# Kernel tuning notes

Hardware: AMD Instinct MI355X
Metric: run time of the kernel (lower is better)

The kernel has to match this reference:

```python
import jax, jax.numpy as jnp
import numpy as np
import math

_DENSE_LOCAL_W = 64
_DYADIC = [96, 128, 192, 256, 384, 512, 768, 1024, 1536]
OFFSETS = sorted(set(range(0, _DENSE_LOCAL_W + 1)) | set(_DYADIC))  # 74 offsets

B, N, D, H = 1, 2048, 1024, 16
HD = D // H


def setup_inputs() -> dict:
    key = jax.random.key(0)
    ks = jax.random.split(key, 8)
    s = 1.0 / math.sqrt(D)
    x = jax.random.normal(ks[0], (B, N, D), dtype=jnp.float32)
    Wqkv = jax.random.uniform(ks[1], (3 * D, D), jnp.float32, -s, s)
    bqkv = jax.random.uniform(ks[2], (3 * D,), jnp.float32, -s, s)
    Wgate = jax.random.uniform(ks[3], (D, D), jnp.float32, -s, s)
    bgate = jax.random.uniform(ks[4], (D,), jnp.float32, -s, s)
    Wout = jax.random.uniform(ks[5], (D, D), jnp.float32, -s, s)
    bout = jax.random.uniform(ks[6], (D,), jnp.float32, -s, s)
    # pos_bias init exactly as in the module: -log(1+delta) * alpha_h, shape (O, H)
    alphas = jnp.linspace(0.2, 2.0, H)
    deltas = jnp.array([math.log(1.0 + d) for d in OFFSETS], dtype=jnp.float32)
    pos_bias = -deltas[:, None] * alphas[None, :]
    offsets = jnp.array(OFFSETS, dtype=jnp.int32)
    return {"x": x, "Wqkv": Wqkv, "bqkv": bqkv, "Wgate": Wgate, "bgate": bgate,
            "Wout": Wout, "bout": bout, "pos_bias": pos_bias, "offsets": offsets}


def reference(x, Wqkv, bqkv, Wgate, bgate, Wout, bout, pos_bias, offsets):
    Bx, Nx, Dx = x.shape
    qkv = x @ Wqkv.T + bqkv                       # (B, N, 3D)
    q, k, v = jnp.split(qkv, 3, axis=-1)
    q = q.reshape(Bx, Nx, H, HD).transpose(0, 2, 1, 3)  # (B, H, N, HD)
    k = k.reshape(Bx, Nx, H, HD).transpose(0, 2, 1, 3)
    v = v.reshape(Bx, Nx, H, HD).transpose(0, 2, 1, 3)
    scale = HD ** -0.5

    # gather shifted K/V: position n attends to n - delta for each fixed offset
    n_idx = jnp.arange(Nx, dtype=jnp.int32)[:, None]      # (N, 1)
    idx = n_idx - offsets[None, :]                        # (N, O)
    valid = idx >= 0                                      # (N, O)
    idx_c = jnp.clip(idx, 0, Nx - 1)
    K_all = k[:, :, idx_c, :]                             # (B, H, N, O, HD)
    V_all = v[:, :, idx_c, :]

    scores = jnp.einsum('bhnd,bhnod->bhno', q, K_all) * scale
    scores = scores + pos_bias.T[None, :, None, :]        # (1, H, 1, O)
    scores = jnp.where(valid[None, None], scores, -jnp.inf)
    alpha = jax.nn.softmax(scores, axis=-1)               # (B, H, N, O)
    out = jnp.einsum('bhno,bhnod->bhnd', alpha, V_all)    # (B, H, N, HD)

    flat = out.transpose(0, 2, 1, 3).reshape(Bx, Nx, Dx)  # (B, N, D)
    gate = jax.nn.sigmoid(x @ Wgate.T + bgate)
    return (flat * gate) @ Wout.T + bout                  # dropout = identity (eval)
```

## Files before the change

### kernel.cpp

```cpp
#include <hip/hip_runtime.h>
#include <hip/hip_bf16.h>

#define SEQ_N 2048
#define DIM   1024
#define NHEAD 16
#define HDIM  64
#define LDQ   4096
#define NOFF  74
#define NDENSE 65
#define NJ    224
#define NT    16
#define PST   232
#define QST   88

typedef __attribute__((ext_vector_type(8)))  __bf16 bv8;
typedef __attribute__((ext_vector_type(4)))  __bf16 bv4;
typedef __attribute__((ext_vector_type(4)))  float  f32x4;
typedef __attribute__((ext_vector_type(16))) float  f32x16;

typedef __attribute__((address_space(3))) void as3_void;
typedef __attribute__((address_space(1))) void as1_void;

__device__ __forceinline__ void async16(const void* g, void* l) {
  __builtin_amdgcn_global_load_lds((as1_void*)(unsigned long long)g,
                                   (as3_void*)l, 16, 0, 0);
}

#define E1 (SEQ_N * DIM)
#define E2 (E1 + 3 * DIM * DIM)
#define E3 (E2 + DIM * DIM)
#define E4 (E3 + DIM * DIM)
__global__ __launch_bounds__(256) void cvt_all(
    const float* __restrict__ x, const float* __restrict__ wqkv,
    const float* __restrict__ wgate, const float* __restrict__ wout,
    __bf16* __restrict__ dst) {
  long i = ((long)blockIdx.x * 256 + threadIdx.x) * 8;
  if (i >= E4) return;
  const float* s; long o;
  if (i < E1)      { s = x;     o = i; }
  else if (i < E2) { s = wqkv;  o = i - E1; }
  else if (i < E3) { s = wgate; o = i - E2; }
  else             { s = wout;  o = i - E3; }
  float4 v0 = *(const float4*)(s + o);
  float4 v1 = *(const float4*)(s + o + 4);
  bv8 ov;
  ov[0] = (__bf16)v0.x; ov[1] = (__bf16)v0.y; ov[2] = (__bf16)v0.z; ov[3] = (__bf16)v0.w;
  ov[4] = (__bf16)v1.x; ov[5] = (__bf16)v1.y; ov[6] = (__bf16)v1.z; ov[7] = (__bf16)v1.w;
  *(bv8*)(dst + i) = ov;
}

template <int BM_, int BN_, int KT, int GX, int GY, typename OutT>
__global__ __launch_bounds__(256, 4) void gemm_bt(
    const __bf16* __restrict__ A, const __bf16* __restrict__ B1,
    const __bf16* __restrict__ B2, const float* __restrict__ bias1,
    const float* __restrict__ bias2, int Nsplit,
    OutT* __restrict__ C, int ldc, int K) {
  __shared__ __attribute__((aligned(16))) __bf16 Asm[BM_ * KT];
  __shared__ __attribute__((aligned(16))) __bf16 Bsm[BN_ * KT];
  constexpr int NI   = BM_ / 64;
  constexpr int NJ32 = BN_ / 64;
  constexpr int CA = BM_ * KT / 8;
  constexpr int CB = BN_ * KT / 8;
  constexpr int CPR = KT / 8;

  const int tid  = threadIdx.x;
  const int lane = tid & 63;
  const int wave = tid >> 6;
  const int wr = wave >> 1, wc = wave & 1;
  const int m31 = lane & 31;
  const int h1  = lane >> 5;
  const int l7  = lane & 7;

  constexpr int NWG = GX * GY;
  const int bid  = blockIdx.y * GX + blockIdx.x;
  const int work = (bid & 7) * (NWG >> 3) + (bid >> 3);
  const int bn0 = (work / GY) * BN_;
  const int bm0 = (work % GY) * BM_;

  const __bf16* Bp;
  const float* biasp;
  if (bn0 < Nsplit) { Bp = B1 + (size_t)bn0 * K;            biasp = bias1 + bn0; }
  else              { Bp = B2 + (size_t)(bn0 - Nsplit) * K; biasp = bias2 + (bn0 - Nsplit); }
  const __bf16* Ap = A + (size_t)bm0 * K;

  f32x16 acc[NI][NJ32] = {};

  for (int kt = 0; kt < K; kt += KT) {
    __syncthreads();
#pragma unroll
    for (int c0 = 0; c0 < CA + CB; c0 += 256) {
      int c = c0 + tid;
      if (c < CA) {
        int rr = c / CPR, qq = c % CPR;
        int qs = qq ^ (rr & 7);
        async16(Ap + (size_t)rr * K + kt + qs * 8, Asm + c * 8);
      } else {
        int cb = c - CA;
        int rr = cb / CPR, qq = cb % CPR;
        int qs = qq ^ (rr & 7);
        async16(Bp + (size_t)rr * K + kt + qs * 8, Bsm + cb * 8);
      }
    }
    __syncthreads();

#pragma unroll
    for (int kk = 0; kk < KT / 16; ++kk) {
      const int qs = ((kk * 2 + h1) ^ l7) * 8;
      bv8 af[NI], bfr[NJ32];
#pragma unroll
      for (int i = 0; i < NI; ++i)
        af[i] = *(const bv8*)(Asm + (wr * (BM_ / 2) + i * 32 + m31) * KT + qs);
#pragma unroll
      for (int j = 0; j < NJ32; ++j)
        bfr[j] = *(const bv8*)(Bsm + (wc * (BN_ / 2) + j * 32 + m31) * KT + qs);
#pragma unroll
      for (int i = 0; i < NI; ++i)
#pragma unroll
        for (int j = 0; j < NJ32; ++j)
          acc[i][j] = __builtin_amdgcn_mfma_f32_32x32x16_bf16(af[i], bfr[j], acc[i][j], 0, 0, 0);
    }
  }

#pragma unroll
  for (int i = 0; i < NI; ++i) {
#pragma unroll
    for (int j = 0; j < NJ32; ++j) {
      int ccol = wc * (BN_ / 2) + j * 32 + m31;
      float b = biasp[ccol];
#pragma unroll
      for (int reg = 0; reg < 16; ++reg) {
        int row = bm0 + wr * (BM_ / 2) + i * 32 + (reg & 3) + 8 * (reg >> 2) + 4 * h1;
        C[(size_t)row * ldc + bn0 + ccol] = (OutT)(acc[i][j][reg] + b);
      }
    }
  }
}

#define BKT 128

template <int GX, int GY, typename OutT>
__global__ __launch_bounds__(256) void gemm_bt64(
    const __bf16* __restrict__ A, const __bf16* __restrict__ B,
    const float* __restrict__ bias, OutT* __restrict__ C, int ldc, int K) {
  __shared__ __attribute__((aligned(16))) __bf16 Asm[64 * BKT];
  __shared__ __attribute__((aligned(16))) __bf16 Bsm[64 * BKT];
  constexpr int CM = 64 * BKT / 8;
  constexpr int CPR = BKT / 8;

  const int tid  = threadIdx.x;
  const int lane = tid & 63;
  const int wave = tid >> 6;
  const int wr = wave >> 1, wc = wave & 1;
  const int m31 = lane & 31;
  const int h1  = lane >> 5;
  const int l7  = lane & 7;

  constexpr int NWG = GX * GY;
  const int bid  = blockIdx.y * GX + blockIdx.x;
  const int work = (bid & 7) * (NWG >> 3) + (bid >> 3);
  const int bn0 = (work / GY) * 64;
  const int bm0 = (work % GY) * 64;

  const __bf16* Ap = A + (size_t)bm0 * K;
  const __bf16* Bp = B + (size_t)bn0 * K;
  const float* biasp = bias + bn0;

  f32x16 acc = {};

  for (int kt = 0; kt < K; kt += BKT) {
    __syncthreads();
#pragma unroll
    for (int c0 = 0; c0 < CM; c0 += 256) {
      int c = c0 + tid;
      int rr = c / CPR, qq = c % CPR;
      int qs = qq ^ (rr & 7);
      async16(Ap + (size_t)rr * K + kt + qs * 8, Asm + c * 8);
      async16(Bp + (size_t)rr * K + kt + qs * 8, Bsm + c * 8);
    }
    __syncthreads();

#pragma unroll
    for (int kk = 0; kk < BKT / 16; ++kk) {
      const int qs = ((kk * 2 + h1) ^ l7) * 8;
      bv8 a = *(const bv8*)(Asm + (wr * 32 + m31) * BKT + qs);
      bv8 b = *(const bv8*)(Bsm + (wc * 32 + m31) * BKT + qs);
      acc = __builtin_amdgcn_mfma_f32_32x32x16_bf16(a, b, acc, 0, 0, 0);
    }
  }

  {
    int ccol = wc * 32 + m31;
    float b = biasp[ccol];
#pragma unroll
    for (int reg = 0; reg < 16; ++reg) {
      int row = bm0 + wr * 32 + (reg & 3) + 8 * (reg >> 2) + 4 * h1;
      C[(size_t)row * ldc + bn0 + ccol] = (OutT)(acc[reg] + b);
    }
  }
}

__global__ __launch_bounds__(256) void attn_mfma(
    const __bf16* __restrict__ qkv,
    const float* __restrict__ pos_bias,
    const int* __restrict__ offsets,
    __bf16* __restrict__ fg) {
  const int n0 = (blockIdx.x >> 4) * NT;
  const int h  = blockIdx.x & 15;
  const int tid = threadIdx.x;
  const int lane = tid & 63;
  const int w = tid >> 6;
  const int fr = lane & 15, fq = lane >> 4;
  const int fr7 = fr & 7;

  __shared__ __attribute__((aligned(16))) __bf16 KVbuf[NJ * HDIM];
  __shared__ __attribute__((aligned(16))) __bf16 Qbuf[NT * QST];
  __shared__ __attribute__((aligned(16))) float  Sbuf[NT][80];
  __shared__ __attribute__((aligned(16))) __bf16 Pd[NT * PST];
  __shared__ float inv_l[NT];

  const int ch = lane & 7;
  const int rowin = lane >> 3;

  if (tid < 128) {
    int ni = tid >> 3, cq = tid & 7;
    bv8 q = *(const bv8*)(qkv + (size_t)(n0 + ni) * LDQ + h * HDIM + cq * 8);
    *(bv8*)(Qbuf + ni * QST + cq * 8) = q;
  }
#pragma unroll
  for (int c0 = 0; c0 < NT * PST / 8; c0 += 256) {
    int c = c0 + tid;
    if (c < NT * PST / 8) *(uint4*)(Pd + c * 8) = make_uint4(0, 0, 0, 0);
  }
  {
    int chs = ch ^ rowin;
#pragma unroll
    for (int it = 0; it < 7; ++it) {
      int jbase = it * 32 + w * 8;
      int j = jbase + rowin;
      int g;
      if (j < 80) g = n0 - 64 + j;
      else { int jj = j - 80; g = n0 - offsets[NDENSE + (jj >> 4)] + (jj & 15); }
      if (g < 0) g = 0;
      async16(qkv + (size_t)g * LDQ + DIM + h * HDIM + chs * 8,
              KVbuf + jbase * HDIM + lane * 8);
    }
  }
  __syncthreads();

  for (int jb = w; jb < 14; jb += 4) {
    f32x4 acc = {};
#pragma unroll
    for (int kk = 0; kk < 2; ++kk) {
      bv8 a = *(const bv8*)(Qbuf + fr * QST + kk * 32 + fq * 8);
      bv8 b = *(const bv8*)(KVbuf + (jb * 16 + fr) * HDIM + ((kk * 4 + fq) ^ fr7) * 8);
      acc = __builtin_amdgcn_mfma_f32_16x16x32_bf16(a, b, acc, 0, 0, 0);
    }
    int j = jb * 16 + fr;
    if (jb < 5) {
      bool gvalid = (n0 - 64 + j) >= 0;
#pragma unroll
      for (int r = 0; r < 4; ++r) {
        int ni = fq * 4 + r;
        int o = ni + 64 - j;
        if (o >= 0 && o < NDENSE)
          Sbuf[ni][o] = gvalid ? acc[r] : -3.0e38f;
      }
    } else {
      int jj = j - 80;
      int s = jj >> 4, tni = jj & 15;
      int r = tni - fq * 4;
      if (r >= 0 && r < 4) {
        bool gvalid = (n0 + tni - offsets[NDENSE + s]) >= 0;
        Sbuf[tni][NDENSE + s] = gvalid ? acc[r] : -3.0e38f;
      }
    }
  }
  __syncthreads();

  {
#pragma unroll
    for (int it = 0; it < 7; ++it) {
      int jbase = it * 32 + w * 8;
      int jv = jbase + (lane >> 5) * 4 + ((lane >> 1) & 3);
      int dv = ((lane >> 3) & 3) * 16 + (lane & 1) * 8;
      int g;
      if (jv < 80) g = n0 - 64 + jv;
      else { int jj = jv - 80; g = n0 - offsets[NDENSE + (jj >> 4)] + (jj & 15); }
      if (g < 0) g = 0;
      async16(qkv + (size_t)g * LDQ + 2 * DIM + h * HDIM + dv,
              KVbuf + jbase * HDIM + lane * 8);
    }
  }

  {
    int t = tid & 15, ni = tid >> 4;
    float sc5[5];
    float m = -3.0e38f;
#pragma unroll
    for (int k = 0; k < 5; ++k) {
      int o = t + k * 16;
      float v = -3.0e38f;
      if (o < NOFF) {
        float raw = Sbuf[ni][o];
        if (raw > -1.0e38f) v = raw * 0.125f + pos_bias[o * NHEAD + h];
      }
      sc5[k] = v;
      m = fmaxf(m, v);
    }
#pragma unroll
    for (int d = 1; d < 16; d <<= 1) m = fmaxf(m, __shfl_xor(m, d));
    float sum = 0.f;
#pragma unroll
    for (int k = 0; k < 5; ++k) {
      int o = t + k * 16;
      if (o < NOFF && sc5[k] > -1.0e38f) {
        float e = __expf(sc5[k] - m);
        sum += e;
        int j = (o < NDENSE) ? (ni + 64 - o) : (80 + (o - NDENSE) * 16 + ni);
        Pd[ni * PST + j] = (__bf16)e;
      }
    }
#pragma unroll
    for (int d = 1; d < 16; d <<= 1) sum += __shfl_xor(sum, d);
    if (t == 0) inv_l[ni] = 1.f / sum;
  }
  __syncthreads();

  {
    const int db = w;
    const unsigned vb0 = (unsigned)(size_t)(as3_void*)KVbuf
                       + fq * 1024 + db * 128 + fr * 8;
    f32x4 acc = {};
#pragma unroll
    for (int kt = 0; kt < 7; ++kt) {
      bv8 a = *(const bv8*)(Pd + fr * PST + kt * 32 + fq * 8);
      bv4 lo, hi;
      asm volatile("ds_read_b64_tr_b16 %0, %2 offset:%3\n\t"
                   "ds_read_b64_tr_b16 %1, %2 offset:%4\n\t"
                   "s_waitcnt lgkmcnt(0)"
                   : "=&v"(lo), "=&v"(hi)
                   : "v"(vb0), "i"(kt * 4096), "i"(kt * 4096 + 512));
      bv8 b;
#pragma unroll
      for (int jj = 0; jj < 4; ++jj) { b[jj] = lo[jj]; b[4 + jj] = hi[jj]; }
      acc = __builtin_amdgcn_mfma_f32_16x16x32_bf16(a, b, acc, 0, 0, 0);
    }
    int d = db * 16 + fr;
#pragma unroll
    for (int r = 0; r < 4; ++r) {
      int ni = fq * 4 + r;
      float o = acc[r] * inv_l[ni];
      float gp = (float)qkv[(size_t)(n0 + ni) * LDQ + 3 * DIM + h * HDIM + d];
      float gate = 1.f / (1.f + __expf(-gp));
      fg[(size_t)(n0 + ni) * DIM + h * HDIM + d] = (__bf16)(o * gate);
    }
  }
}

extern "C" void kernel_launch(void* const* d_in, const int* in_sizes, int n_in,
                              void* d_out, int out_size, void* d_ws, size_t ws_size,
                              hipStream_t stream) {
  const float* x        = (const float*)d_in[0];
  const float* Wqkv     = (const float*)d_in[1];
  const float* bqkv     = (const float*)d_in[2];
  const float* Wgate    = (const float*)d_in[3];
  const float* bgate    = (const float*)d_in[4];
  const float* Wout     = (const float*)d_in[5];
  const float* bout     = (const float*)d_in[6];
  const float* pos_bias = (const float*)d_in[7];
  const int*   offsets  = (const int*)d_in[8];
  float* out = (float*)d_out;

  __bf16* xb       = (__bf16*)d_ws;
  __bf16* Wqkvb    = xb    + (size_t)SEQ_N * DIM;
  __bf16* Wgateb   = Wqkvb + (size_t)3 * DIM * DIM;
  __bf16* Woutb    = Wgateb + (size_t)DIM * DIM;
  __bf16* qkvg     = Woutb + (size_t)DIM * DIM;
  __bf16* flatgate = qkvg + (size_t)SEQ_N * LDQ;

  cvt_all<<<dim3(E4 / 2048), dim3(256), 0, stream>>>(x, Wqkv, Wgate, Wout, xb);

  gemm_bt<64, 128, 64, 32, 32, __bf16>
      <<<dim3(32, 32), dim3(256), 0, stream>>>(
      xb, Wqkvb, Wgateb, bqkv, bgate, 3 * DIM, qkvg, LDQ, DIM);

  attn_mfma<<<dim3((SEQ_N / NT) * NHEAD), dim3(256), 0, stream>>>(
      qkvg, pos_bias, offsets, flatgate);

  gemm_bt64<16, 32, float><<<dim3(DIM / 64, SEQ_N / 64), dim3(256), 0, stream>>>(
      flatgate, Woutb, bout, out, DIM, DIM);
}
```

Measured before the change: 144.4 us.

## Double-buffer GEMM K loop and enlarge tiles with a unified GEMM template

Replaces both GEMM kernels with a single templated kernel that double-buffers shared memory, issuing async global-to-LDS loads for the next K tile while computing the current one, so each step needs one barrier instead of two. The QKV/gate GEMM moves to 128x256 tiles with 512 threads, and the output projection moves from 64x64 to 64x128 tiles. The intent is to hide load latency and raise data reuse per tile. In exchange, the larger tiles produce fewer workgroups (256 per GEMM) and more LDS per block, which lowers occupancy and may leave CUs underused.

After: 143.9 us. No clear change (-0.3%).

```diff
diff --git a/kernel.cpp b/kernel.cpp
--- a/kernel.cpp
+++ b/kernel.cpp
@@ -49,24 +49,27 @@
   *(bv8*)(dst + i) = ov;
 }
 
-template <int BM_, int BN_, int KT, int GX, int GY, typename OutT>
-__global__ __launch_bounds__(256, 4) void gemm_bt(
+template <int BM_, int BN_, int KT_, int WM, int WN, int GX, int GY, typename OutT>
+__global__ __launch_bounds__(WM * WN * 64) void gemm_bt2(
     const __bf16* __restrict__ A, const __bf16* __restrict__ B1,
     const __bf16* __restrict__ B2, const float* __restrict__ bias1,
     const float* __restrict__ bias2, int Nsplit,
     OutT* __restrict__ C, int ldc, int K) {
-  __shared__ __attribute__((aligned(16))) __bf16 Asm[BM_ * KT];
-  __shared__ __attribute__((aligned(16))) __bf16 Bsm[BN_ * KT];
-  constexpr int NI   = BM_ / 64;
-  constexpr int NJ32 = BN_ / 64;
-  constexpr int CA = BM_ * KT / 8;
-  constexpr int CB = BN_ * KT / 8;
-  constexpr int CPR = KT / 8;
+  constexpr int NTHR = WM * WN * 64;
+  constexpr int NI  = BM_ / (WM * 32);
+  constexpr int NJ_ = BN_ / (WN * 32);
+  constexpr int CA = BM_ * KT_ / 8;
+  constexpr int CB = BN_ * KT_ / 8;
+  constexpr int CT = CA + CB;
+  constexpr int CPR = KT_ / 8;
+  static_assert(CA % NTHR == 0 && CT % NTHR == 0, "stage divisibility");
+
+  __shared__ __attribute__((aligned(16))) __bf16 smem[2][(BM_ + BN_) * KT_];
 
   const int tid  = threadIdx.x;
   const int lane = tid & 63;
   const int wave = tid >> 6;
-  const int wr = wave >> 1, wc = wave & 1;
+  const int wm = wave / WN, wn = wave % WN;
   const int m31 = lane & 31;
   const int h1  = lane >> 5;
   const int l7  = lane & 7;
@@ -83,118 +86,71 @@
   else              { Bp = B2 + (size_t)(bn0 - Nsplit) * K; biasp = bias2 + (bn0 - Nsplit); }
   const __bf16* Ap = A + (size_t)bm0 * K;
 
-  f32x16 acc[NI][NJ32] = {};
-
-  for (int kt = 0; kt < K; kt += KT) {
+  f32x16 acc[NI][NJ_] = {};
+
+#define STAGE_STEP(KTOFF, SEL)                                            \
+  {                                                                       \
+    _Pragma("unroll")                                                     \
+    for (int c0 = 0; c0 < CT; c0 += NTHR) {                               \
+      int c = c0 + tid;                                                   \
+      if (c < CA) {                                                       \
+        int rr = c / CPR, qq = c % CPR;                                   \
+        int qs = qq ^ (rr & 7);                                           \
+        async16(Ap + (size_t)rr * K + (KTOFF) + qs * 8,                   \
+                &smem[SEL][0] + c * 8);                                   \
+      } else {                                                            \
+        int cb = c - CA;                                                  \
+        int rr = cb / CPR, qq = cb % CPR;                                 \
+        int qs = qq ^ (rr & 7);                                           \
+        async16(Bp + (size_t)rr * K + (KTOFF) + qs * 8,                   \
+                &smem[SEL][BM_ * KT_] + cb * 8);                          \
+      }                                                                   \
+    }                                                                     \
+  }
+
+  STAGE_STEP(0, 0)
+  __syncthreads();
+
+  const int NSTEP = K / KT_;
+  int sel = 0;
+  for (int t = 0; t < NSTEP; ++t) {
+    if (t + 1 < NSTEP) STAGE_STEP((t + 1) * KT_, sel ^ 1)
+
+#pragma unroll
+    for (int kk = 0; kk < KT_ / 16; ++kk) {
+      const int qs = ((kk * 2 + h1) ^ l7) * 8;
+      bv8 af[NI], bfr[NJ_];
+#pragma unroll
+      for (int i = 0; i < NI; ++i)
+        af[i] = *(const bv8*)(&smem[sel][0] +
+                              (wm * (BM_ / WM) + i * 32 + m31) * KT_ + qs);
+#pragma unroll
+      for (int j = 0; j < NJ_; ++j)
+        bfr[j] = *(const bv8*)(&smem[sel][BM_ * KT_] +
+                               (wn * (BN_ / WN) + j * 32 + m31) * KT_ + qs);
+#pragma unroll
+      for (int i = 0; i < NI; ++i)
+#pragma unroll
+        for (int j = 0; j < NJ_; ++j)
+          acc[i][j] = __builtin_amdgcn_mfma_f32_32x32x16_bf16(af[i], bfr[j], acc[i][j], 0, 0, 0);
+    }
+
     __syncthreads();
-#pragma unroll
-    for (int c0 = 0; c0 < CA + CB; c0 += 256) {
-      int c = c0 + tid;
-      if (c < CA) {
-        int rr = c / CPR, qq = c % CPR;
-        int qs = qq ^ (rr & 7);
-        async16(Ap + (size_t)rr * K + kt + qs * 8, Asm + c * 8);
-      } else {
-        int cb = c - CA;
-        int rr = cb / CPR, qq = cb % CPR;
-        int qs = qq ^ (rr & 7);
-        async16(Bp + (size_t)rr * K + kt + qs * 8, Bsm + cb * 8);
-      }
-    }
-    __syncthreads();
-
-#pragma unroll
-    for (int kk = 0; kk < KT / 16; ++kk) {
-      const int qs = ((kk * 2 + h1) ^ l7) * 8;
-      bv8 af[NI], bfr[NJ32];
-#pragma unroll
-      for (int i = 0; i < NI; ++i)
-        af[i] = *(const bv8*)(Asm + (wr * (BM_ / 2) + i * 32 + m31) * KT + qs);
-#pragma unroll
-      for (int j = 0; j < NJ32; ++j)
-        bfr[j] = *(const bv8*)(Bsm + (wc * (BN_ / 2) + j * 32 + m31) * KT + qs);
-#pragma unroll
-      for (int i = 0; i < NI; ++i)
-#pragma unroll
-        for (int j = 0; j < NJ32; ++j)
-          acc[i][j] = __builtin_amdgcn_mfma_f32_32x32x16_bf16(af[i], bfr[j], acc[i][j], 0, 0, 0);
-    }
-  }
+    sel ^= 1;
+  }
+#undef STAGE_STEP
 
 #pragma unroll
   for (int i = 0; i < NI; ++i) {
 #pragma unroll
-    for (int j = 0; j < NJ32; ++j) {
-      int ccol = wc * (BN_ / 2) + j * 32 + m31;
+    for (int j = 0; j < NJ_; ++j) {
+      int ccol = wn * (BN_ / WN) + j * 32 + m31;
       float b = biasp[ccol];
 #pragma unroll
       for (int reg = 0; reg < 16; ++reg) {
-        int row = bm0 + wr * (BM_ / 2) + i * 32 + (reg & 3) + 8 * (reg >> 2) + 4 * h1;
+        int row = bm0 + wm * (BM_ / WM) + i * 32 + (reg & 3) + 8 * (reg >> 2) + 4 * h1;
         C[(size_t)row * ldc + bn0 + ccol] = (OutT)(acc[i][j][reg] + b);
       }
-    }
-  }
-}
-
-#define BKT 128
-
-template <int GX, int GY, typename OutT>
-__global__ __launch_bounds__(256) void gemm_bt64(
-    const __bf16* __restrict__ A, const __bf16* __restrict__ B,
-    const float* __restrict__ bias, OutT* __restrict__ C, int ldc, int K) {
-  __shared__ __attribute__((aligned(16))) __bf16 Asm[64 * BKT];
-  __shared__ __attribute__((aligned(16))) __bf16 Bsm[64 * BKT];
-  constexpr int CM = 64 * BKT / 8;
-  constexpr int CPR = BKT / 8;
-
-  const int tid  = threadIdx.x;
-  const int lane = tid & 63;
-  const int wave = tid >> 6;
-  const int wr = wave >> 1, wc = wave & 1;
-  const int m31 = lane & 31;
-  const int h1  = lane >> 5;
-  const int l7  = lane & 7;
-
-  constexpr int NWG = GX * GY;
-  const int bid  = blockIdx.y * GX + blockIdx.x;
-  const int work = (bid & 7) * (NWG >> 3) + (bid >> 3);
-  const int bn0 = (work / GY) * 64;
-  const int bm0 = (work % GY) * 64;
-
-  const __bf16* Ap = A + (size_t)bm0 * K;
-  const __bf16* Bp = B + (size_t)bn0 * K;
-  const float* biasp = bias + bn0;
-
-  f32x16 acc = {};
-
-  for (int kt = 0; kt < K; kt += BKT) {
-    __syncthreads();
-#pragma unroll
-    for (int c0 = 0; c0 < CM; c0 += 256) {
-      int c = c0 + tid;
-      int rr = c / CPR, qq = c % CPR;
-      int qs = qq ^ (rr & 7);
-      async16(Ap + (size_t)rr * K + kt + qs * 8, Asm + c * 8);
-      async16(Bp + (size_t)rr * K + kt + qs * 8, Bsm + c * 8);
-    }
-    __syncthreads();
-
-#pragma unroll
-    for (int kk = 0; kk < BKT / 16; ++kk) {
-      const int qs = ((kk * 2 + h1) ^ l7) * 8;
-      bv8 a = *(const bv8*)(Asm + (wr * 32 + m31) * BKT + qs);
-      bv8 b = *(const bv8*)(Bsm + (wc * 32 + m31) * BKT + qs);
-      acc = __builtin_amdgcn_mfma_f32_32x32x16_bf16(a, b, acc, 0, 0, 0);
-    }
-  }
-
-  {
-    int ccol = wc * 32 + m31;
-    float b = biasp[ccol];
-#pragma unroll
-    for (int reg = 0; reg < 16; ++reg) {
-      int row = bm0 + wr * 32 + (reg & 3) + 8 * (reg >> 2) + 4 * h1;
-      C[(size_t)row * ldc + bn0 + ccol] = (OutT)(acc[reg] + b);
     }
   }
 }
@@ -380,13 +336,14 @@
 
   cvt_all<<<dim3(E4 / 2048), dim3(256), 0, stream>>>(x, Wqkv, Wgate, Wout, xb);
 
-  gemm_bt<64, 128, 64, 32, 32, __bf16>
-      <<<dim3(32, 32), dim3(256), 0, stream>>>(
+  gemm_bt2<128, 256, 64, 2, 4, 16, 16, __bf16>
+      <<<dim3(16, 16), dim3(512), 0, stream>>>(
       xb, Wqkvb, Wgateb, bqkv, bgate, 3 * DIM, qkvg, LDQ, DIM);
 
   attn_mfma<<<dim3((SEQ_N / NT) * NHEAD), dim3(256), 0, stream>>>(
       qkvg, pos_bias, offsets, flatgate);
 
-  gemm_bt64<16, 32, float><<<dim3(DIM / 64, SEQ_N / 64), dim3(256), 0, stream>>>(
-      flatgate, Woutb, bout, out, DIM, DIM);
-}
+  gemm_bt2<64, 128, 64, 2, 2, 8, 32, float>
+      <<<dim3(8, 32), dim3(256), 0, stream>>>(
+      flatgate, Woutb, Woutb, bout, bout, DIM, out, DIM, DIM);
+}
```
